# Kernel optimization log

Measured on AMD Instinct MI355X. Metric: run time of the kernel, lower is better.

## Reference

```python
import jax, jax.numpy as jnp
import numpy as np

N, CT, C, L, H, W, HEAD, GROUPS = 4, 512, 512, 256, 64, 64, 16, 16


def setup_inputs() -> dict:
    key = jax.random.key(0)
    ks = jax.random.split(key, 8)
    d_in_g = C // GROUPS
    return {
        "feature": jax.random.normal(ks[0], (N, C, H, W), dtype=jnp.float32),
        "token": jax.random.normal(ks[1], (N, CT, L), dtype=jnp.float32),
        # conv1x1_1d value/key projections: weight [C_out, C_in]
        "Wv": jax.random.normal(ks[2], (C, CT), dtype=jnp.float32) * (1.0 / np.sqrt(CT)),
        "bv": jnp.zeros((C,), dtype=jnp.float32),
        "Wk": jax.random.normal(ks[3], (C, CT), dtype=jnp.float32) * (1.0 / np.sqrt(CT)),
        "bk": jnp.zeros((C,), dtype=jnp.float32),
        # grouped conv1x1_2d query projection: weight [groups, C_out/g, C_in/g]
        "Wq": jax.random.normal(ks[4], (GROUPS, d_in_g, d_in_g), dtype=jnp.float32) * (1.0 / np.sqrt(d_in_g)),
        "bq": jnp.zeros((C,), dtype=jnp.float32),
    }


def reference(feature, token, Wv, bv, Wk, bk, Wq, bq):
    h = HEAD
    d = C // h              # per-head dim
    S = H * W               # query positions
    # value / key: 1x1 conv1d == matmul over channel dim
    proj_v = (jnp.einsum('oc,ncl->nol', Wv, token) + bv[None, :, None]).reshape(N, h, d, L)
    proj_k = (jnp.einsum('oc,ncl->nol', Wk, token) + bk[None, :, None]).reshape(N, h, d, L)
    # query: grouped 1x1 conv2d (padding=0; see notes) == per-group matmul
    f_g = feature.reshape(N, GROUPS, C // GROUPS, S)
    q = jnp.einsum('goi,ngis->ngos', Wq, f_g).reshape(N, C, S) + bq[None, :, None]
    proj_q = q.reshape(N, h, d, S).transpose(0, 1, 3, 2)  # [N, h, S, d]
    scale = 1.0 / np.sqrt(C / h)
    scores = jnp.einsum('nhsd,nhdl->nhsl', proj_q, proj_k) * scale  # [N,h,S,L]
    proj_coef = jax.nn.softmax(scores, axis=3)
    proj = jnp.einsum('nhdl,nhsl->nhds', proj_v, proj_coef)  # [N,h,d,S]
    return feature + proj.reshape(N, C, H, W)
```

## Files before the change

kernel.cpp:

```cpp
#include <hip/hip_runtime.h>

typedef float f32x4 __attribute__((ext_vector_type(4)));
typedef short bf16x8 __attribute__((ext_vector_type(8)));
typedef __bf16 bf2 __attribute__((ext_vector_type(2)));
typedef unsigned short u16;
typedef unsigned int u32;

#define CT_ 512
#define C_ 512
#define L_ 256
#define S_ 4096
#define D_ 32

static __device__ __forceinline__ u16 f2bf(float x) {
    union { __bf16 h; u16 u; } v; v.h = (__bf16)x; return v.u;
}
static __device__ __forceinline__ u32 packbf(float a, float b) {
    union { bf2 h; u32 u; } v;
    v.h[0] = (__bf16)a; v.h[1] = (__bf16)b;
    return v.u;
}

__global__ __launch_bounds__(256) void prep_all(const float* __restrict__ Wv,
                                                const float* __restrict__ Wk,
                                                const float* __restrict__ token,
                                                u16* __restrict__ wbf,
                                                u16* __restrict__ tokT) {
    __shared__ float tile[32][33];
    int bx = blockIdx.x;
    int t = threadIdx.x;
    if (bx < 256) {
        int idx = (bx * 256 + t) * 8;
        const float* src = (idx < 262144) ? (Wv + idx) : (Wk + (idx - 262144));
        float4 a = *(const float4*)src;
        float4 b = *(const float4*)(src + 4);
        uint4 o;
        o.x = packbf(a.x, a.y);
        o.y = packbf(a.z, a.w);
        o.z = packbf(b.x, b.y);
        o.w = packbf(b.z, b.w);
        *(uint4*)(wbf + idx) = o;
    } else {
        int b2 = bx - 256;
        int ct_t = b2 & 15, l_t = (b2 >> 4) & 7, n = b2 >> 7;
        int r = t >> 3, c4 = (t & 7) * 4;
        const float* src = token + ((size_t)n * CT_ + ct_t * 32 + r) * L_ + l_t * 32 + c4;
        float4 v = *(const float4*)src;
        tile[r][c4] = v.x; tile[r][c4 + 1] = v.y; tile[r][c4 + 2] = v.z; tile[r][c4 + 3] = v.w;
        __syncthreads();
        uint2 o;
        o.x = packbf(tile[c4][r],     tile[c4 + 1][r]);
        o.y = packbf(tile[c4 + 2][r], tile[c4 + 3][r]);
        *(uint2*)(tokT + ((size_t)n * L_ + l_t * 32 + r) * CT_ + ct_t * 32 + c4) = o;
    }
}

__global__ __launch_bounds__(64) void kv_gemm(const u16* __restrict__ Wv_bf,
                                              const u16* __restrict__ Wk_bf,
                                              const u16* __restrict__ tokT,
                                              const float* __restrict__ bv,
                                              const float* __restrict__ bk,
                                              u16* __restrict__ V_hs,
                                              u16* __restrict__ KT_hs) {
    int bx = blockIdx.x;
    int l_t = bx & 7, c_t = (bx >> 3) & 15, kv = (bx >> 7) & 1, n = bx >> 8;
    const u16* W = kv ? Wk_bf : Wv_bf;
    const float* bias = kv ? bk : bv;
    int c0 = c_t * 32, l0 = l_t * 32;
    int lane = threadIdx.x;
    int lr = lane & 15, g = lane >> 4;

    const f32x4 fz = {0.f, 0.f, 0.f, 0.f};
    f32x4 acc[2][2] = {{fz, fz}, {fz, fz}};

    const u16* Abase = W + (size_t)(c0 + lr) * CT_ + g * 8;
    const u16* Bbase = tokT + ((size_t)n * L_ + l0 + lr) * CT_ + g * 8;

#pragma unroll
    for (int k = 0; k < 16; ++k) {
        bf16x8 a0 = *(const bf16x8*)(Abase + k * 32);
        bf16x8 a1 = *(const bf16x8*)(Abase + (size_t)16 * CT_ + k * 32);
        bf16x8 b0 = *(const bf16x8*)(Bbase + k * 32);
        bf16x8 b1 = *(const bf16x8*)(Bbase + (size_t)16 * CT_ + k * 32);
        acc[0][0] = __builtin_amdgcn_mfma_f32_16x16x32_bf16(a0, b0, acc[0][0], 0, 0, 0);
        acc[0][1] = __builtin_amdgcn_mfma_f32_16x16x32_bf16(a0, b1, acc[0][1], 0, 0, 0);
        acc[1][0] = __builtin_amdgcn_mfma_f32_16x16x32_bf16(a1, b0, acc[1][0], 0, 0, 0);
        acc[1][1] = __builtin_amdgcn_mfma_f32_16x16x32_bf16(a1, b1, acc[1][1], 0, 0, 0);
    }

    float bb[2][4];
#pragma unroll
    for (int ci = 0; ci < 2; ++ci)
#pragma unroll
        for (int r = 0; r < 4; ++r) bb[ci][r] = bias[c0 + ci * 16 + g * 4 + r];

    if (kv == 0) {
#pragma unroll
        for (int ci = 0; ci < 2; ++ci)
#pragma unroll
            for (int jt = 0; jt < 2; ++jt) {
                int o = jt * 16 + lr;
                int c = o >> 2, q = o & 3;
                int ip = ((c >> 2) & 1) | ((c & 3) << 1);
                int dst_l = l0 + ip * 4 + q;
#pragma unroll
                for (int r = 0; r < 4; ++r) {
                    int d = ci * 16 + g * 4 + r;
                    V_hs[(((size_t)n * 16 + c_t) * D_ + d) * L_ + dst_l] =
                        f2bf(acc[ci][jt][r] + bb[ci][r]);
                }
            }
    } else {
#pragma unroll
        for (int jt = 0; jt < 2; ++jt) {
            int l = l0 + jt * 16 + lr;
#pragma unroll
            for (int ci = 0; ci < 2; ++ci) {
                uint2 o;
                o.x = packbf(acc[ci][jt][0] + bb[ci][0], acc[ci][jt][1] + bb[ci][1]);
                o.y = packbf(acc[ci][jt][2] + bb[ci][2], acc[ci][jt][3] + bb[ci][3]);
                *(uint2*)(KT_hs + (((size_t)n * 16 + c_t) * L_ + l) * D_
                          + g * 8 + ci * 4) = o;
            }
        }
    }
}

__global__ __launch_bounds__(256, 4) void attn(const float* __restrict__ feature,
                                               const float* __restrict__ Wq,
                                               const float* __restrict__ bq,
                                               const u16* __restrict__ V_hs,
                                               const u16* __restrict__ KT_hs,
                                               float* __restrict__ out) {
    __shared__ u16 KT_lds[256][40];
    __shared__ u16 V_lds[32][296];

    int bx = blockIdx.x;
    int sb = bx & 31, h = (bx >> 5) & 15, n = bx >> 9;
    int s_base = sb * 128;
    int t = threadIdx.x;
    int w = t >> 6, lane = t & 63, lr = lane & 15, g = lane >> 4;
    const f32x4 fz = {0.f, 0.f, 0.f, 0.f};

    {
        const u16* kbase = KT_hs + ((size_t)n * 16 + h) * (L_ * D_);
#pragma unroll
        for (int i = 0; i < 4; ++i) {
            uint4 v = *(const uint4*)(kbase + ((size_t)i * 256 + t) * 8);
            *(uint4*)&KT_lds[i * 64 + (t >> 2)][(t & 3) * 8] = v;
        }
    }
    {
        const u16* vbase = V_hs + ((size_t)n * 16 + h) * (D_ * L_);
#pragma unroll
        for (int i = 0; i < 4; ++i) {
            uint4 v = *(const uint4*)(vbase + ((size_t)i * 256 + t) * 8);
            *(uint4*)&V_lds[i * 8 + (t >> 5)][(t & 31) * 8] = v;
        }
    }

    const float scale = 0.17677669529663687f * 1.4426950408889634f;
    union { u32 d[4]; bf16x8 v; } wqf[2];
#pragma unroll
    for (int dt = 0; dt < 2; ++dt) {
        const float* wsrc = Wq + ((size_t)h * D_ + dt * 16 + lr) * D_ + g * 8;
        float4 w0 = *(const float4*)wsrc;
        float4 w1 = *(const float4*)(wsrc + 4);
        wqf[dt].d[0] = packbf(w0.x * scale, w0.y * scale);
        wqf[dt].d[1] = packbf(w0.z * scale, w0.w * scale);
        wqf[dt].d[2] = packbf(w1.x * scale, w1.y * scale);
        wqf[dt].d[3] = packbf(w1.z * scale, w1.w * scale);
    }
    float bqs[2][4];
#pragma unroll
    for (int dt = 0; dt < 2; ++dt)
#pragma unroll
        for (int r = 0; r < 4; ++r)
            bqs[dt][r] = bq[h * D_ + dt * 16 + g * 4 + r] * scale;

    const float* fb = feature + ((size_t)n * C_ + h * D_) * S_ + s_base + w * 16 + lr;
    float f[8];
#pragma unroll
    for (int j = 0; j < 8; ++j) f[j] = fb[(size_t)(g * 8 + j) * S_];

    __syncthreads();

#pragma unroll
    for (int tile = 0; tile < 2; ++tile) {
        int s0 = s_base + tile * 64;

        union { u32 d[4]; bf16x8 v; } au;
#pragma unroll
        for (int k = 0; k < 4; ++k) au.d[k] = packbf(f[2 * k], f[2 * k + 1]);
        if (tile == 0) {
#pragma unroll
            for (int j = 0; j < 8; ++j) f[j] = fb[(size_t)(g * 8 + j) * S_ + 64];
        }

        f32x4 aq0 = __builtin_amdgcn_mfma_f32_16x16x32_bf16(wqf[0].v, au.v, fz, 0, 0, 0);
        f32x4 aq1 = __builtin_amdgcn_mfma_f32_16x16x32_bf16(wqf[1].v, au.v, fz, 0, 0, 0);
        union { u32 d[4]; bf16x8 v; } qb;
        qb.d[0] = packbf(aq0[0] + bqs[0][0], aq0[1] + bqs[0][1]);
        qb.d[1] = packbf(aq0[2] + bqs[0][2], aq0[3] + bqs[0][3]);
        qb.d[2] = packbf(aq1[0] + bqs[1][0], aq1[1] + bqs[1][1]);
        qb.d[3] = packbf(aq1[2] + bqs[1][2], aq1[3] + bqs[1][3]);

        f32x4 accs[16];
#pragma unroll
        for (int lt = 0; lt < 16; ++lt) {
            bf16x8 a = *(const bf16x8*)&KT_lds[lt * 16 + lr][g * 8];
            accs[lt] = __builtin_amdgcn_mfma_f32_16x16x32_bf16(a, qb.v, fz, 0, 0, 0);
        }

        float s4[4] = {0.f, 0.f, 0.f, 0.f};
#pragma unroll
        for (int lt = 0; lt < 16; ++lt) {
#pragma unroll
            for (int r = 0; r < 4; ++r) {
                float e = __builtin_amdgcn_exp2f(accs[lt][r]);
                accs[lt][r] = e;
                s4[r] += e;
            }
        }
        float sum = (s4[0] + s4[1]) + (s4[2] + s4[3]);
        sum += __shfl_xor(sum, 16, 64);
        sum += __shfl_xor(sum, 32, 64);
        float inv_own = __builtin_amdgcn_rcpf(sum);

        f32x4 acco[2] = {fz, fz};
#pragma unroll
        for (int tc = 0; tc < 8; ++tc) {
            union { u32 d[4]; bf16x8 v; } pa;
#pragma unroll
            for (int j = 0; j < 4; ++j)
                pa.d[j] = packbf(accs[2 * tc + (j >> 1)][(j & 1) * 2],
                                 accs[2 * tc + (j >> 1)][(j & 1) * 2 + 1]);
#pragma unroll
            for (int dt = 0; dt < 2; ++dt) {
                bf16x8 vb = *(const bf16x8*)&V_lds[dt * 16 + lr][tc * 32 + g * 8];
                acco[dt] = __builtin_amdgcn_mfma_f32_16x16x32_bf16(pa.v, vb, acco[dt], 0, 0, 0);
            }
        }

        float inv4[4];
#pragma unroll
        for (int r = 0; r < 4; ++r)
            inv4[r] = __shfl(inv_own, (lane & 48) | (g * 4 + r), 64);
#pragma unroll
        for (int dt = 0; dt < 2; ++dt) {
            size_t off = ((size_t)n * C_ + h * D_ + dt * 16 + lr) * S_
                       + s0 + w * 16 + g * 4;
            float4 fe = *(const float4*)(feature + off);
            float4 o;
            o.x = fe.x + acco[dt][0] * inv4[0];
            o.y = fe.y + acco[dt][1] * inv4[1];
            o.z = fe.z + acco[dt][2] * inv4[2];
            o.w = fe.w + acco[dt][3] * inv4[3];
            *(float4*)(out + off) = o;
        }

        if (tile == 0) __syncthreads();
    }
}

extern "C" void kernel_launch(void* const* d_in, const int* in_sizes, int n_in,
                              void* d_out, int out_size, void* d_ws, size_t ws_size,
                              hipStream_t stream) {
    const float* feature = (const float*)d_in[0];
    const float* token   = (const float*)d_in[1];
    const float* Wv      = (const float*)d_in[2];
    const float* bv      = (const float*)d_in[3];
    const float* Wk      = (const float*)d_in[4];
    const float* bk      = (const float*)d_in[5];
    const float* Wq      = (const float*)d_in[6];
    const float* bq      = (const float*)d_in[7];
    float* out = (float*)d_out;

    u16* ws16  = (u16*)d_ws;
    u16* Wv_bf = ws16;
    u16* Wk_bf = Wv_bf + 262144;
    u16* tokT  = Wk_bf + 262144;
    u16* V_hs  = tokT + 524288;
    u16* KT_hs = V_hs + 524288;

    prep_all<<<dim3(768), dim3(256), 0, stream>>>(Wv, Wk, token, Wv_bf, tokT);
    kv_gemm<<<dim3(1024), dim3(64), 0, stream>>>(Wv_bf, Wk_bf, tokT, bv, bk, V_hs, KT_hs);
    attn<<<dim3(2048), dim3(256), 0, stream>>>(feature, Wq, bq, V_hs, KT_hs, out);
}
```

Measured before the change: 41.79 us.

## Swizzle blocks across XCDs, prefetch feature loads, split MFMA accumulator chains

Block indices in both kv_gemm and attn are remapped so consecutive blocks (which land on different XCDs) share the same batch and head group, aiming for better L2 locality of the K/V and weight data. In attn, both feature tiles are loaded up front and the residual feature loads are issued before the QK MFMAs to hide latency. The query bias is folded into the MFMA accumulator input, and the PV accumulation is split into two independent chains to shorten MFMA dependency stalls. The cost is higher register pressure, which could hurt occupancy under the (256,4) launch bound.

```diff
diff --git a/kernel.cpp b/kernel.cpp
--- a/kernel.cpp
+++ b/kernel.cpp
@@ -63,7 +63,9 @@
                                               u16* __restrict__ V_hs,
                                               u16* __restrict__ KT_hs) {
     int bx = blockIdx.x;
-    int l_t = bx & 7, c_t = (bx >> 3) & 15, kv = (bx >> 7) & 1, n = bx >> 8;
+    int xcd = bx & 7, slot = bx >> 3;
+    int l_t = slot & 7, hb = (slot >> 3) & 1, kv = (slot >> 4) & 1, n = slot >> 5;
+    int c_t = (hb << 3) | xcd;
     const u16* W = kv ? Wk_bf : Wv_bf;
     const float* bias = kv ? bk : bv;
     int c0 = c_t * 32, l0 = l_t * 32;
@@ -136,7 +138,9 @@
     __shared__ u16 V_lds[32][296];
 
     int bx = blockIdx.x;
-    int sb = bx & 31, h = (bx >> 5) & 15, n = bx >> 9;
+    int xcd = bx & 7, slot = bx >> 3;
+    int sb = slot & 31, hb = (slot >> 5) & 1, n = slot >> 6;
+    int h = (hb << 3) | xcd;
     int s_base = sb * 128;
     int t = threadIdx.x;
     int w = t >> 6, lane = t & 63, lr = lane & 15, g = lane >> 4;
@@ -171,17 +175,19 @@
         wqf[dt].d[2] = packbf(w1.x * scale, w1.y * scale);
         wqf[dt].d[3] = packbf(w1.z * scale, w1.w * scale);
     }
-    float bqs[2][4];
+    f32x4 bqc[2];
 #pragma unroll
     for (int dt = 0; dt < 2; ++dt)
 #pragma unroll
         for (int r = 0; r < 4; ++r)
-            bqs[dt][r] = bq[h * D_ + dt * 16 + g * 4 + r] * scale;
+            bqc[dt][r] = bq[h * D_ + dt * 16 + g * 4 + r] * scale;
 
     const float* fb = feature + ((size_t)n * C_ + h * D_) * S_ + s_base + w * 16 + lr;
-    float f[8];
-#pragma unroll
-    for (int j = 0; j < 8; ++j) f[j] = fb[(size_t)(g * 8 + j) * S_];
+    float f0[8], f1[8];
+#pragma unroll
+    for (int j = 0; j < 8; ++j) f0[j] = fb[(size_t)(g * 8 + j) * S_];
+#pragma unroll
+    for (int j = 0; j < 8; ++j) f1[j] = fb[(size_t)(g * 8 + j) * S_ + 64];
 
     __syncthreads();
 
@@ -191,19 +197,22 @@
 
         union { u32 d[4]; bf16x8 v; } au;
 #pragma unroll
-        for (int k = 0; k < 4; ++k) au.d[k] = packbf(f[2 * k], f[2 * k + 1]);
-        if (tile == 0) {
-#pragma unroll
-            for (int j = 0; j < 8; ++j) f[j] = fb[(size_t)(g * 8 + j) * S_ + 64];
-        }
-
-        f32x4 aq0 = __builtin_amdgcn_mfma_f32_16x16x32_bf16(wqf[0].v, au.v, fz, 0, 0, 0);
-        f32x4 aq1 = __builtin_amdgcn_mfma_f32_16x16x32_bf16(wqf[1].v, au.v, fz, 0, 0, 0);
+        for (int k = 0; k < 4; ++k)
+            au.d[k] = tile == 0 ? packbf(f0[2 * k], f0[2 * k + 1])
+                                : packbf(f1[2 * k], f1[2 * k + 1]);
+
+        f32x4 aq0 = __builtin_amdgcn_mfma_f32_16x16x32_bf16(wqf[0].v, au.v, bqc[0], 0, 0, 0);
+        f32x4 aq1 = __builtin_amdgcn_mfma_f32_16x16x32_bf16(wqf[1].v, au.v, bqc[1], 0, 0, 0);
         union { u32 d[4]; bf16x8 v; } qb;
-        qb.d[0] = packbf(aq0[0] + bqs[0][0], aq0[1] + bqs[0][1]);
-        qb.d[1] = packbf(aq0[2] + bqs[0][2], aq0[3] + bqs[0][3]);
-        qb.d[2] = packbf(aq1[0] + bqs[1][0], aq1[1] + bqs[1][1]);
-        qb.d[3] = packbf(aq1[2] + bqs[1][2], aq1[3] + bqs[1][3]);
+        qb.d[0] = packbf(aq0[0], aq0[1]);
+        qb.d[1] = packbf(aq0[2], aq0[3]);
+        qb.d[2] = packbf(aq1[0], aq1[1]);
+        qb.d[3] = packbf(aq1[2], aq1[3]);
+
+        size_t eoff0 = ((size_t)n * C_ + h * D_ + lr) * S_ + s0 + w * 16 + g * 4;
+        size_t eoff1 = eoff0 + (size_t)16 * S_;
+        float4 fe0 = *(const float4*)(feature + eoff0);
+        float4 fe1 = *(const float4*)(feature + eoff1);
 
         f32x4 accs[16];
 #pragma unroll
@@ -227,7 +236,7 @@
         sum += __shfl_xor(sum, 32, 64);
         float inv_own = __builtin_amdgcn_rcpf(sum);
 
-        f32x4 acco[2] = {fz, fz};
+        f32x4 acc4[2][2] = {{fz, fz}, {fz, fz}};
 #pragma unroll
         for (int tc = 0; tc < 8; ++tc) {
             union { u32 d[4]; bf16x8 v; } pa;
@@ -238,26 +247,29 @@
 #pragma unroll
             for (int dt = 0; dt < 2; ++dt) {
                 bf16x8 vb = *(const bf16x8*)&V_lds[dt * 16 + lr][tc * 32 + g * 8];
-                acco[dt] = __builtin_amdgcn_mfma_f32_16x16x32_bf16(pa.v, vb, acco[dt], 0, 0, 0);
+                acc4[dt][tc & 1] =
+                    __builtin_amdgcn_mfma_f32_16x16x32_bf16(pa.v, vb, acc4[dt][tc & 1], 0, 0, 0);
             }
         }
+        f32x4 acco[2];
+        acco[0] = acc4[0][0] + acc4[0][1];
+        acco[1] = acc4[1][0] + acc4[1][1];
 
         float inv4[4];
 #pragma unroll
         for (int r = 0; r < 4; ++r)
             inv4[r] = __shfl(inv_own, (lane & 48) | (g * 4 + r), 64);
-#pragma unroll
-        for (int dt = 0; dt < 2; ++dt) {
-            size_t off = ((size_t)n * C_ + h * D_ + dt * 16 + lr) * S_
-                       + s0 + w * 16 + g * 4;
-            float4 fe = *(const float4*)(feature + off);
-            float4 o;
-            o.x = fe.x + acco[dt][0] * inv4[0];
-            o.y = fe.y + acco[dt][1] * inv4[1];
-            o.z = fe.z + acco[dt][2] * inv4[2];
-            o.w = fe.w + acco[dt][3] * inv4[3];
-            *(float4*)(out + off) = o;
-        }
+        float4 o0, o1;
+        o0.x = fe0.x + acco[0][0] * inv4[0];
+        o0.y = fe0.y + acco[0][1] * inv4[1];
+        o0.z = fe0.z + acco[0][2] * inv4[2];
+        o0.w = fe0.w + acco[0][3] * inv4[3];
+        o1.x = fe1.x + acco[1][0] * inv4[0];
+        o1.y = fe1.y + acco[1][1] * inv4[1];
+        o1.z = fe1.z + acco[1][2] * inv4[2];
+        o1.w = fe1.w + acco[1][3] * inv4[3];
+        *(float4*)(out + eoff0) = o0;
+        *(float4*)(out + eoff1) = o1;
 
         if (tile == 0) __syncthreads();
     }
```

New measurement: 43.87 us. +5.0%, slower.
